# Kernel tuning notes

Measured on AMD Instinct MI355X. Metric: run time of the kernel, lower is better.

Reference implementation:

```python
import jax, jax.numpy as jnp
import numpy as np


def setup_inputs() -> dict:
    key = jax.random.key(0)
    k1, k2, k3, k4 = jax.random.split(key, 4)
    B, L1, L2, H, A = 64, 512, 512, 1024, 1024
    reps_lt = jax.random.normal(k1, (B, L1, H), dtype=jnp.float32)
    reps_rt = jax.random.normal(k2, (B, L2, H), dtype=jnp.float32)
    mask_lt = jnp.ones((B, L1), dtype=jnp.float32)
    mask_rt = jnp.ones((B, L2), dtype=jnp.float32)
    # Keras 'uniform' initializer ~ U(-0.05, 0.05); scale similarly
    attn_w1 = jax.random.uniform(k3, (H, A), dtype=jnp.float32, minval=-0.05, maxval=0.05)
    diagonal_W = jax.random.uniform(k4, (1, 1, A), dtype=jnp.float32, minval=-0.05, maxval=0.05)
    return {
        "reps_lt": reps_lt,
        "reps_rt": reps_rt,
        "mask_lt": mask_lt,
        "mask_rt": mask_rt,
        "attn_w1": attn_w1,
        "diagonal_W": diagonal_W,
    }


def reference(reps_lt, reps_rt, mask_lt, mask_rt, attn_w1, diagonal_W):
    # Projections: the original does expand_dims + broadcast multiply + sum,
    # which is mathematically a matmul over the hidden dim.
    # attn_w2 aliases attn_w1 because hidden dims are equal.
    attn_lt = jnp.tanh(jnp.einsum('blh,ha->bla', reps_lt, attn_w1))  # [B,L1,A]
    attn_rt = jnp.tanh(jnp.einsum('brh,ha->bra', reps_rt, attn_w1))  # [B,L2,A]
    attn_lt = attn_lt * diagonal_W                                   # diagonal bilinear scale
    # batch_dot([B,L1,A], [B,A,L2]) -> [B,L1,L2]
    attn_value = jnp.einsum('bla,bra->blr', attn_lt, attn_rt)
    # mask (multiplicative, as in original) before softmax
    attn_value = attn_value * mask_lt[:, :, None] * mask_rt[:, None, :]
    attn_prob = jax.nn.softmax(attn_value, axis=-1)
    # mask again after softmax
    attn_prob = attn_prob * mask_lt[:, :, None] * mask_rt[:, None, :]
    return attn_prob
```

## Files before the change

kernel.cpp:

```cpp
#include <hip/hip_runtime.h>
#include <hip/hip_bf16.h>

#define B_ 64
#define L_ 512
#define H_ 1024
#define A_ 1024

typedef short bf16x8 __attribute__((ext_vector_type(8)));
typedef float f32x4 __attribute__((ext_vector_type(4)));

__device__ __forceinline__ void gld16(const void* g, void* l) {
  __builtin_amdgcn_global_load_lds((const __attribute__((address_space(1))) void*)g,
                                   (__attribute__((address_space(3))) void*)l, 16, 0, 0);
}

__device__ __forceinline__ unsigned short f2bf(float f) {
  unsigned u = __builtin_bit_cast(unsigned, f);
  u = (u + 0x7fffu + ((u >> 16) & 1u)) >> 16;
  return (unsigned short)u;
}

__device__ __forceinline__ unsigned short cvtbf(float f) {
  __hip_bfloat16 b = __float2bfloat16(f);
  return __builtin_bit_cast(unsigned short, b);
}

__device__ __forceinline__ float fast_tanh(float x) {
  float e = __expf(2.f * x);
  float r = __builtin_amdgcn_rcpf(e + 1.f);
  return __builtin_fmaf(-2.f, r, 1.f);
}

__global__ __launch_bounds__(256) void cvt_kernel(const float* __restrict__ lt,
                                                  const float* __restrict__ rt,
                                                  unsigned short* __restrict__ xb) {
  const size_t NC = (size_t)B_ * L_ * H_ / 8;
  size_t stride = (size_t)gridDim.x * blockDim.x;
  for (size_t c = (size_t)blockIdx.x * blockDim.x + threadIdx.x; c < 2 * NC; c += stride) {
    const float* src = (c < NC) ? (lt + c * 8) : (rt + (c - NC) * 8);
    float4 v0 = ((const float4*)src)[0];
    float4 v1 = ((const float4*)src)[1];
    bf16x8 o;
    o[0] = (short)cvtbf(v0.x); o[1] = (short)cvtbf(v0.y);
    o[2] = (short)cvtbf(v0.z); o[3] = (short)cvtbf(v0.w);
    o[4] = (short)cvtbf(v1.x); o[5] = (short)cvtbf(v1.y);
    o[6] = (short)cvtbf(v1.z); o[7] = (short)cvtbf(v1.w);
    *(bf16x8*)(xb + c * 8) = o;
  }
}

__global__ __launch_bounds__(256) void wtrans_kernel(const float* __restrict__ W,
                                                     unsigned short* __restrict__ Wt) {
  __shared__ float tile[32][33];
  int tx = threadIdx.x & 31, ty = threadIdx.x >> 5;
  int a0 = (blockIdx.x & 31) << 5, h0 = (blockIdx.x >> 5) << 5;
#pragma unroll
  for (int i = 0; i < 4; ++i) {
    int h = ty + i * 8;
    tile[h][tx] = W[(size_t)(h0 + h) * A_ + a0 + tx];
  }
  __syncthreads();
#pragma unroll
  for (int i = 0; i < 4; ++i) {
    int a = ty + i * 8;
    Wt[(size_t)(a0 + a) * H_ + h0 + tx] = f2bf(tile[tx][a]);
  }
}

__global__ __launch_bounds__(512, 2) void proj8_kernel(
    const unsigned short* __restrict__ Xb, const unsigned short* __restrict__ Wt,
    const float* __restrict__ diag, unsigned short* __restrict__ Pb) {
  __shared__ unsigned short As[2][256 * 64];
  __shared__ unsigned short Bs[2][256 * 64];
  int t = threadIdx.x;
  int lane = t & 63, wave = t >> 6;
  int wr = wave >> 2, wc = wave & 3;
  int l15 = lane & 15, l4 = lane >> 4;

  int bid = (int)blockIdx.x;
  int x = bid & 7, k = bid >> 3;
  int mt = x + 8 * (k >> 2);
  int nt = k & 3;
  int mrow0 = mt << 8, ncol0 = nt << 8;
  int isLt = (mt < 128);

  int rs = t >> 3, ss = t & 7;
  const unsigned short* gA = Xb + (size_t)(mrow0 + rs) * H_ + ((ss ^ (rs & 7)) << 3);
  const unsigned short* gB = Wt + (size_t)(ncol0 + rs) * H_ + ((ss ^ (rs & 7)) << 3);
  int lofs = (rs * 8 + ss) * 8;

#define STG_A(buf, h, kt_) {                                              \
    const unsigned short* g_ = gA + (size_t)(h) * 128 * H_ + (kt_) * 64;  \
    gld16(g_, &As[buf][(h) * 8192 + lofs]);                               \
    gld16(g_ + (size_t)64 * H_, &As[buf][(h) * 8192 + 4096 + lofs]); }
#define STG_B(buf, h, kt_) {                                              \
    const unsigned short* g_ = gB + (size_t)(h) * 128 * H_ + (kt_) * 64;  \
    gld16(g_, &Bs[buf][(h) * 8192 + lofs]);                               \
    gld16(g_ + (size_t)64 * H_, &Bs[buf][(h) * 8192 + 4096 + lofs]); }

  int rd0 = (l4 ^ (l15 & 7)) * 8;
  int rd1 = ((4 + l4) ^ (l15 & 7)) * 8;

  f32x4 acc[8][4] = {};
  bf16x8 bq[4][2];

#define LOAD_BQ(buf) { _Pragma("unroll") for (int ni = 0; ni < 4; ++ni) {  \
    int brow = wc * 64 + ni * 16 + l15;                                    \
    bq[ni][0] = *(const bf16x8*)&Bs[buf][brow * 64 + rd0];                 \
    bq[ni][1] = *(const bf16x8*)&Bs[buf][brow * 64 + rd1]; } }

#define PHASE(q, buf, STAGE_OP, CKPT) {                                    \
    bf16x8 aq0, aq1, aq2, aq3;                                             \
    { int ar = wr * 128 + (q) * 32 + l15;                                  \
      aq0 = *(const bf16x8*)&As[buf][ar * 64 + rd0];                       \
      aq1 = *(const bf16x8*)&As[buf][ar * 64 + rd1];                       \
      aq2 = *(const bf16x8*)&As[buf][(ar + 16) * 64 + rd0];                \
      aq3 = *(const bf16x8*)&As[buf][(ar + 16) * 64 + rd1]; }              \
    STAGE_OP;                                                              \
    asm volatile("s_barrier" ::: "memory");                                \
    __builtin_amdgcn_s_setprio(1);                                         \
    _Pragma("unroll") for (int ni = 0; ni < 4; ++ni) {                     \
      acc[(q)*2][ni] = __builtin_amdgcn_mfma_f32_16x16x32_bf16(            \
          aq0, bq[ni][0], acc[(q)*2][ni], 0, 0, 0);                        \
      acc[(q)*2][ni] = __builtin_amdgcn_mfma_f32_16x16x32_bf16(            \
          aq1, bq[ni][1], acc[(q)*2][ni], 0, 0, 0);                        \
      acc[(q)*2+1][ni] = __builtin_amdgcn_mfma_f32_16x16x32_bf16(          \
          aq2, bq[ni][0], acc[(q)*2+1][ni], 0, 0, 0);                      \
      acc[(q)*2+1][ni] = __builtin_amdgcn_mfma_f32_16x16x32_bf16(          \
          aq3, bq[ni][1], acc[(q)*2+1][ni], 0, 0, 0); }                    \
    __builtin_amdgcn_s_setprio(0);                                         \
    if (CKPT) asm volatile("s_waitcnt vmcnt(4)" ::: "memory");             \
    asm volatile("s_barrier" ::: "memory"); }

  STG_B(0, 0, 0); STG_B(0, 1, 0);
  STG_A(0, 0, 0); STG_A(0, 1, 0);
  STG_B(1, 0, 1); STG_B(1, 1, 1);
  asm volatile("s_waitcnt vmcnt(4)" ::: "memory");
  asm volatile("s_barrier" ::: "memory");

  for (int i = 0; i < 8; ++i) {
    int kt1 = 2 * i + 1;
    int kt2 = (2 * i + 2) & 15, kt3 = (2 * i + 3) & 15;
    LOAD_BQ(0);
    PHASE(0, 0, STG_A(1, 0, kt1), 0);
    PHASE(1, 0, STG_A(1, 1, kt1), 0);
    PHASE(2, 0, STG_B(0, 0, kt2), 0);
    PHASE(3, 0, STG_B(0, 1, kt2), 1);
    LOAD_BQ(1);
    PHASE(0, 1, STG_A(0, 0, kt2), 0);
    PHASE(1, 1, STG_A(0, 1, kt2), 0);
    PHASE(2, 1, STG_B(1, 0, kt3), 0);
    PHASE(3, 1, STG_B(1, 1, kt3), 1);
  }
#undef PHASE
#undef LOAD_BQ
#undef STG_A
#undef STG_B

#pragma unroll
  for (int mi = 0; mi < 8; ++mi) {
#pragma unroll
    for (int ni = 0; ni < 4; ++ni) {
      int col = ncol0 + wc * 64 + ni * 16 + l15;
      float d = isLt ? diag[col] : 1.0f;
#pragma unroll
      for (int rr = 0; rr < 4; ++rr) {
        int row = mrow0 + wr * 128 + mi * 16 + l4 * 4 + rr;
        Pb[(size_t)row * A_ + col] = f2bf(fast_tanh(acc[mi][ni][rr]) * d);
      }
    }
  }
}

__global__ __launch_bounds__(256) void score_kernel(
    const unsigned short* __restrict__ Plt, const unsigned short* __restrict__ Prt,
    const float* __restrict__ mask_lt, const float* __restrict__ mask_rt,
    float* __restrict__ out) {
  __shared__ unsigned short As[128 * 64];
  __shared__ unsigned short Bs[128 * 64];
  int t = threadIdx.x;
  int lane = t & 63, wave = t >> 6;
  int wr = wave >> 1, wc = wave & 1;
  int l15 = lane & 15, l4 = lane >> 4;

  int bid = (int)blockIdx.x;
  int x = bid & 7, k = bid >> 3;
  int atile = x + 8 * (k >> 2);
  int b = atile >> 2, tm = atile & 3, tn = k & 3;

  const unsigned short* Abase = Plt + (size_t)b * L_ * A_ + (size_t)(tm * 128) * A_;
  const unsigned short* Bbase = Prt + (size_t)b * L_ * A_ + (size_t)(tn * 128) * A_;

  const unsigned short* asrc[4];
  const unsigned short* bsrc[4];
  int dst[4];
#pragma unroll
  for (int i = 0; i < 4; ++i) {
    int c = i * 256 + t;
    int r = c >> 3, kc = c & 7;
    int sc = (kc ^ (r & 7)) * 8;
    asrc[i] = &Abase[(size_t)r * A_ + sc];
    bsrc[i] = &Bbase[(size_t)r * A_ + sc];
    dst[i] = c * 8;
  }
  int swz0 = ((0 * 4 + l4) ^ (l15 & 7)) * 8;
  int swz1 = ((1 * 4 + l4) ^ (l15 & 7)) * 8;

  f32x4 acc[4][4] = {};
  for (int kt = 0; kt < A_ / 64; ++kt) {
    int k0 = kt * 64;
    __syncthreads();
#pragma unroll
    for (int i = 0; i < 4; ++i) {
      gld16(asrc[i] + k0, &As[dst[i]]);
      gld16(bsrc[i] + k0, &Bs[dst[i]]);
    }
    __syncthreads();
#pragma unroll
    for (int kk = 0; kk < 2; ++kk) {
      int sw = kk ? swz1 : swz0;
      bf16x8 aq[4], bq[4];
#pragma unroll
      for (int mi = 0; mi < 4; ++mi)
        aq[mi] = *(const bf16x8*)&As[(wr * 64 + mi * 16 + l15) * 64 + sw];
#pragma unroll
      for (int ni = 0; ni < 4; ++ni)
        bq[ni] = *(const bf16x8*)&Bs[(wc * 64 + ni * 16 + l15) * 64 + sw];
#pragma unroll
      for (int mi = 0; mi < 4; ++mi)
#pragma unroll
        for (int ni = 0; ni < 4; ++ni)
          acc[mi][ni] = __builtin_amdgcn_mfma_f32_16x16x32_bf16(aq[mi], bq[ni], acc[mi][ni], 0, 0, 0);
    }
  }
  const float* mlp = mask_lt + b * L_;
  const float* mrp = mask_rt + b * L_;
  float* obase = out + (size_t)b * L_ * L_;
#pragma unroll
  for (int mi = 0; mi < 4; ++mi) {
#pragma unroll
    for (int ni = 0; ni < 4; ++ni) {
      int col = tn * 128 + wc * 64 + ni * 16 + l15;
      float mr = mrp[col];
#pragma unroll
      for (int r = 0; r < 4; ++r) {
        int row = tm * 128 + wr * 64 + mi * 16 + l4 * 4 + r;
        obase[(size_t)row * L_ + col] = acc[mi][ni][r] * mlp[row] * mr;
      }
    }
  }
}

__global__ __launch_bounds__(256) void softmax_kernel(float* __restrict__ out,
                                                      const float* __restrict__ mask_lt,
                                                      const float* __restrict__ mask_rt) {
  int lane = threadIdx.x & 63, wave = threadIdx.x >> 6;
  int row = (int)blockIdx.x * 4 + wave;
  int b = row >> 9;
  float* p = out + (size_t)row * L_;
  float4 v0 = *(const float4*)(p + lane * 8);
  float4 v1 = *(const float4*)(p + lane * 8 + 4);
  float m = fmaxf(fmaxf(fmaxf(v0.x, v0.y), fmaxf(v0.z, v0.w)),
                  fmaxf(fmaxf(v1.x, v1.y), fmaxf(v1.z, v1.w)));
#pragma unroll
  for (int off = 32; off; off >>= 1) m = fmaxf(m, __shfl_xor(m, off));
  float e0 = __expf(v0.x - m), e1 = __expf(v0.y - m), e2 = __expf(v0.z - m), e3 = __expf(v0.w - m);
  float e4 = __expf(v1.x - m), e5 = __expf(v1.y - m), e6 = __expf(v1.z - m), e7 = __expf(v1.w - m);
  float s = ((e0 + e1) + (e2 + e3)) + ((e4 + e5) + (e6 + e7));
#pragma unroll
  for (int off = 32; off; off >>= 1) s += __shfl_xor(s, off);
  float sc = (1.0f / s) * mask_lt[row];
  const float* mrp = mask_rt + (b << 9) + lane * 8;
  float4 mr0 = *(const float4*)mrp;
  float4 mr1 = *(const float4*)(mrp + 4);
  float4 o0 = make_float4(e0 * sc * mr0.x, e1 * sc * mr0.y, e2 * sc * mr0.z, e3 * sc * mr0.w);
  float4 o1 = make_float4(e4 * sc * mr1.x, e5 * sc * mr1.y, e6 * sc * mr1.z, e7 * sc * mr1.w);
  *(float4*)(p + lane * 8) = o0;
  *(float4*)(p + lane * 8 + 4) = o1;
}

extern "C" void kernel_launch(void* const* d_in, const int* in_sizes, int n_in,
                              void* d_out, int out_size, void* d_ws, size_t ws_size,
                              hipStream_t stream) {
  const float* reps_lt = (const float*)d_in[0];
  const float* reps_rt = (const float*)d_in[1];
  const float* mask_lt = (const float*)d_in[2];
  const float* mask_rt = (const float*)d_in[3];
  const float* attn_w1 = (const float*)d_in[4];
  const float* diag    = (const float*)d_in[5];
  float* out = (float*)d_out;

  unsigned short* wt  = (unsigned short*)d_ws;
  unsigned short* pb  = wt + (size_t)H_ * A_;
  unsigned short* xb  = pb + (size_t)B_ * L_ * A_ * 2;
  unsigned short* plt = pb;
  unsigned short* prt = pb + (size_t)B_ * L_ * A_;

  hipLaunchKernelGGL(wtrans_kernel, dim3(1024), dim3(256), 0, stream, attn_w1, wt);
  hipLaunchKernelGGL(cvt_kernel, dim3(8192), dim3(256), 0, stream,
                     reps_lt, reps_rt, xb);
  hipLaunchKernelGGL(proj8_kernel, dim3(1024), dim3(512), 0, stream,
                     xb, wt, diag, pb);
  hipLaunchKernelGGL(score_kernel, dim3(1024), dim3(256), 0, stream,
                     plt, prt, mask_lt, mask_rt, out);
  hipLaunchKernelGGL(softmax_kernel, dim3(8192), dim3(256), 0, stream,
                     out, mask_lt, mask_rt);
}
```

Baseline: 315.3 us.

## Reuse pipelined 256x256 MFMA conveyor for the batched score GEMM

The score GEMM moves from a simple 128x128-tile kernel, which syncs twice per k-step, to the 256x256-tile, 512-thread, double-buffered phased pipeline already used by the projection kernel. The pipeline is factored into a shared macro. Larger tiles halve global/LDS traffic per FLOP and overlap loads with MFMA. The cost is only 256 blocks on a GPU with 256 CUs, so each CU gets a single wave of work and occupancy is low.

```diff
diff --git a/kernel.cpp b/kernel.cpp
--- a/kernel.cpp
+++ b/kernel.cpp
@@ -67,55 +67,23 @@
   }
 }
 
-__global__ __launch_bounds__(512, 2) void proj8_kernel(
-    const unsigned short* __restrict__ Xb, const unsigned short* __restrict__ Wt,
-    const float* __restrict__ diag, unsigned short* __restrict__ Pb) {
-  __shared__ unsigned short As[2][256 * 64];
-  __shared__ unsigned short Bs[2][256 * 64];
-  int t = threadIdx.x;
-  int lane = t & 63, wave = t >> 6;
-  int wr = wave >> 2, wc = wave & 3;
-  int l15 = lane & 15, l4 = lane >> 4;
-
-  int bid = (int)blockIdx.x;
-  int x = bid & 7, k = bid >> 3;
-  int mt = x + 8 * (k >> 2);
-  int nt = k & 3;
-  int mrow0 = mt << 8, ncol0 = nt << 8;
-  int isLt = (mt < 128);
-
-  int rs = t >> 3, ss = t & 7;
-  const unsigned short* gA = Xb + (size_t)(mrow0 + rs) * H_ + ((ss ^ (rs & 7)) << 3);
-  const unsigned short* gB = Wt + (size_t)(ncol0 + rs) * H_ + ((ss ^ (rs & 7)) << 3);
-  int lofs = (rs * 8 + ss) * 8;
-
-#define STG_A(buf, h, kt_) {                                              \
-    const unsigned short* g_ = gA + (size_t)(h) * 128 * H_ + (kt_) * 64;  \
-    gld16(g_, &As[buf][(h) * 8192 + lofs]);                               \
-    gld16(g_ + (size_t)64 * H_, &As[buf][(h) * 8192 + 4096 + lofs]); }
-#define STG_B(buf, h, kt_) {                                              \
-    const unsigned short* g_ = gB + (size_t)(h) * 128 * H_ + (kt_) * 64;  \
-    gld16(g_, &Bs[buf][(h) * 8192 + lofs]);                               \
-    gld16(g_ + (size_t)64 * H_, &Bs[buf][(h) * 8192 + 4096 + lofs]); }
-
-  int rd0 = (l4 ^ (l15 & 7)) * 8;
-  int rd1 = ((4 + l4) ^ (l15 & 7)) * 8;
-
-  f32x4 acc[8][4] = {};
-  bf16x8 bq[4][2];
-
-#define LOAD_BQ(buf) { _Pragma("unroll") for (int ni = 0; ni < 4; ++ni) {  \
+#define STG_FROM(gptr, Ls, buf, h, kt_) {                                  \
+    const unsigned short* g_ = (gptr) + (size_t)(h) * 128 * H_ + (kt_) * 64; \
+    gld16(g_, &Ls[buf][(h) * 8192 + lofs]);                                \
+    gld16(g_ + (size_t)64 * H_, &Ls[buf][(h) * 8192 + 4096 + lofs]); }
+
+#define LOAD_BQ(Bsrc, buf) { _Pragma("unroll") for (int ni = 0; ni < 4; ++ni) { \
     int brow = wc * 64 + ni * 16 + l15;                                    \
-    bq[ni][0] = *(const bf16x8*)&Bs[buf][brow * 64 + rd0];                 \
-    bq[ni][1] = *(const bf16x8*)&Bs[buf][brow * 64 + rd1]; } }
-
-#define PHASE(q, buf, STAGE_OP, CKPT) {                                    \
+    bq[ni][0] = *(const bf16x8*)&Bsrc[buf][brow * 64 + rd0];               \
+    bq[ni][1] = *(const bf16x8*)&Bsrc[buf][brow * 64 + rd1]; } }
+
+#define PHASE(Asrc, q, buf, STAGE_OP, CKPT) {                              \
     bf16x8 aq0, aq1, aq2, aq3;                                             \
     { int ar = wr * 128 + (q) * 32 + l15;                                  \
-      aq0 = *(const bf16x8*)&As[buf][ar * 64 + rd0];                       \
-      aq1 = *(const bf16x8*)&As[buf][ar * 64 + rd1];                       \
-      aq2 = *(const bf16x8*)&As[buf][(ar + 16) * 64 + rd0];                \
-      aq3 = *(const bf16x8*)&As[buf][(ar + 16) * 64 + rd1]; }              \
+      aq0 = *(const bf16x8*)&Asrc[buf][ar * 64 + rd0];                     \
+      aq1 = *(const bf16x8*)&Asrc[buf][ar * 64 + rd1];                     \
+      aq2 = *(const bf16x8*)&Asrc[buf][(ar + 16) * 64 + rd0];              \
+      aq3 = *(const bf16x8*)&Asrc[buf][(ar + 16) * 64 + rd1]; }            \
     STAGE_OP;                                                              \
     asm volatile("s_barrier" ::: "memory");                                \
     __builtin_amdgcn_s_setprio(1);                                         \
@@ -132,30 +100,56 @@
     if (CKPT) asm volatile("s_waitcnt vmcnt(4)" ::: "memory");             \
     asm volatile("s_barrier" ::: "memory"); }
 
-  STG_B(0, 0, 0); STG_B(0, 1, 0);
-  STG_A(0, 0, 0); STG_A(0, 1, 0);
-  STG_B(1, 0, 1); STG_B(1, 1, 1);
-  asm volatile("s_waitcnt vmcnt(4)" ::: "memory");
-  asm volatile("s_barrier" ::: "memory");
-
-  for (int i = 0; i < 8; ++i) {
-    int kt1 = 2 * i + 1;
-    int kt2 = (2 * i + 2) & 15, kt3 = (2 * i + 3) & 15;
-    LOAD_BQ(0);
-    PHASE(0, 0, STG_A(1, 0, kt1), 0);
-    PHASE(1, 0, STG_A(1, 1, kt1), 0);
-    PHASE(2, 0, STG_B(0, 0, kt2), 0);
-    PHASE(3, 0, STG_B(0, 1, kt2), 1);
-    LOAD_BQ(1);
-    PHASE(0, 1, STG_A(0, 0, kt2), 0);
-    PHASE(1, 1, STG_A(0, 1, kt2), 0);
-    PHASE(2, 1, STG_B(1, 0, kt3), 0);
-    PHASE(3, 1, STG_B(1, 1, kt3), 1);
-  }
-#undef PHASE
-#undef LOAD_BQ
-#undef STG_A
-#undef STG_B
+#define CONVEYOR(gA_, gB_)                                                 \
+  STG_FROM(gB_, Bs, 0, 0, 0); STG_FROM(gB_, Bs, 0, 1, 0);                  \
+  STG_FROM(gA_, As, 0, 0, 0); STG_FROM(gA_, As, 0, 1, 0);                  \
+  STG_FROM(gB_, Bs, 1, 0, 1); STG_FROM(gB_, Bs, 1, 1, 1);                  \
+  asm volatile("s_waitcnt vmcnt(4)" ::: "memory");                         \
+  asm volatile("s_barrier" ::: "memory");                                  \
+  for (int i = 0; i < 8; ++i) {                                            \
+    int kt1 = 2 * i + 1;                                                   \
+    int kt2 = (2 * i + 2) & 15, kt3 = (2 * i + 3) & 15;                    \
+    LOAD_BQ(Bs, 0);                                                        \
+    PHASE(As, 0, 0, STG_FROM(gA_, As, 1, 0, kt1), 0);                      \
+    PHASE(As, 1, 0, STG_FROM(gA_, As, 1, 1, kt1), 0);                      \
+    PHASE(As, 2, 0, STG_FROM(gB_, Bs, 0, 0, kt2), 0);                      \
+    PHASE(As, 3, 0, STG_FROM(gB_, Bs, 0, 1, kt2), 1);                      \
+    LOAD_BQ(Bs, 1);                                                        \
+    PHASE(As, 0, 1, STG_FROM(gA_, As, 0, 0, kt2), 0);                      \
+    PHASE(As, 1, 1, STG_FROM(gA_, As, 0, 1, kt2), 0);                      \
+    PHASE(As, 2, 1, STG_FROM(gB_, Bs, 1, 0, kt3), 0);                      \
+    PHASE(As, 3, 1, STG_FROM(gB_, Bs, 1, 1, kt3), 1);                      \
+  }
+
+__global__ __launch_bounds__(512, 2) void proj8_kernel(
+    const unsigned short* __restrict__ Xb, const unsigned short* __restrict__ Wt,
+    const float* __restrict__ diag, unsigned short* __restrict__ Pb) {
+  __shared__ unsigned short As[2][256 * 64];
+  __shared__ unsigned short Bs[2][256 * 64];
+  int t = threadIdx.x;
+  int lane = t & 63, wave = t >> 6;
+  int wr = wave >> 2, wc = wave & 3;
+  int l15 = lane & 15, l4 = lane >> 4;
+
+  int bid = (int)blockIdx.x;
+  int x = bid & 7, k = bid >> 3;
+  int mt = x + 8 * (k >> 2);
+  int nt = k & 3;
+  int mrow0 = mt << 8, ncol0 = nt << 8;
+  int isLt = (mt < 128);
+
+  int rs = t >> 3, ss = t & 7;
+  const unsigned short* gA = Xb + (size_t)(mrow0 + rs) * H_ + ((ss ^ (rs & 7)) << 3);
+  const unsigned short* gB = Wt + (size_t)(ncol0 + rs) * H_ + ((ss ^ (rs & 7)) << 3);
+  int lofs = (rs * 8 + ss) * 8;
+
+  int rd0 = (l4 ^ (l15 & 7)) * 8;
+  int rd1 = ((4 + l4) ^ (l15 & 7)) * 8;
+
+  f32x4 acc[8][4] = {};
+  bf16x8 bq[4][2];
+
+  CONVEYOR(gA, gB);
 
 #pragma unroll
   for (int mi = 0; mi < 8; ++mi) {
@@ -172,80 +166,51 @@
   }
 }
 
-__global__ __launch_bounds__(256) void score_kernel(
-    const unsigned short* __restrict__ Plt, const unsigned short* __restrict__ Prt,
+__global__ __launch_bounds__(512, 2) void score8_kernel(
+    const unsigned short* __restrict__ Pb,
     const float* __restrict__ mask_lt, const float* __restrict__ mask_rt,
     float* __restrict__ out) {
-  __shared__ unsigned short As[128 * 64];
-  __shared__ unsigned short Bs[128 * 64];
+  __shared__ unsigned short As[2][256 * 64];
+  __shared__ unsigned short Bs[2][256 * 64];
   int t = threadIdx.x;
   int lane = t & 63, wave = t >> 6;
-  int wr = wave >> 1, wc = wave & 1;
+  int wr = wave >> 2, wc = wave & 3;
   int l15 = lane & 15, l4 = lane >> 4;
 
   int bid = (int)blockIdx.x;
   int x = bid & 7, k = bid >> 3;
-  int atile = x + 8 * (k >> 2);
-  int b = atile >> 2, tm = atile & 3, tn = k & 3;
-
-  const unsigned short* Abase = Plt + (size_t)b * L_ * A_ + (size_t)(tm * 128) * A_;
-  const unsigned short* Bbase = Prt + (size_t)b * L_ * A_ + (size_t)(tn * 128) * A_;
-
-  const unsigned short* asrc[4];
-  const unsigned short* bsrc[4];
-  int dst[4];
-#pragma unroll
-  for (int i = 0; i < 4; ++i) {
-    int c = i * 256 + t;
-    int r = c >> 3, kc = c & 7;
-    int sc = (kc ^ (r & 7)) * 8;
-    asrc[i] = &Abase[(size_t)r * A_ + sc];
-    bsrc[i] = &Bbase[(size_t)r * A_ + sc];
-    dst[i] = c * 8;
-  }
-  int swz0 = ((0 * 4 + l4) ^ (l15 & 7)) * 8;
-  int swz1 = ((1 * 4 + l4) ^ (l15 & 7)) * 8;
-
-  f32x4 acc[4][4] = {};
-  for (int kt = 0; kt < A_ / 64; ++kt) {
-    int k0 = kt * 64;
-    __syncthreads();
-#pragma unroll
-    for (int i = 0; i < 4; ++i) {
-      gld16(asrc[i] + k0, &As[dst[i]]);
-      gld16(bsrc[i] + k0, &Bs[dst[i]]);
-    }
-    __syncthreads();
-#pragma unroll
-    for (int kk = 0; kk < 2; ++kk) {
-      int sw = kk ? swz1 : swz0;
-      bf16x8 aq[4], bq[4];
-#pragma unroll
-      for (int mi = 0; mi < 4; ++mi)
-        aq[mi] = *(const bf16x8*)&As[(wr * 64 + mi * 16 + l15) * 64 + sw];
-#pragma unroll
-      for (int ni = 0; ni < 4; ++ni)
-        bq[ni] = *(const bf16x8*)&Bs[(wc * 64 + ni * 16 + l15) * 64 + sw];
-#pragma unroll
-      for (int mi = 0; mi < 4; ++mi)
-#pragma unroll
-        for (int ni = 0; ni < 4; ++ni)
-          acc[mi][ni] = __builtin_amdgcn_mfma_f32_16x16x32_bf16(aq[mi], bq[ni], acc[mi][ni], 0, 0, 0);
-    }
-  }
+  int pm = x + 8 * (k >> 1);
+  int b = pm >> 1, mt = pm & 1, nt = k & 1;
+
+  int arow0 = b * 512 + mt * 256;
+  int brow0 = 32768 + b * 512 + nt * 256;
+
+  int rs = t >> 3, ss = t & 7;
+  const unsigned short* gA = Pb + (size_t)(arow0 + rs) * H_ + ((ss ^ (rs & 7)) << 3);
+  const unsigned short* gB = Pb + (size_t)(brow0 + rs) * H_ + ((ss ^ (rs & 7)) << 3);
+  int lofs = (rs * 8 + ss) * 8;
+
+  int rd0 = (l4 ^ (l15 & 7)) * 8;
+  int rd1 = ((4 + l4) ^ (l15 & 7)) * 8;
+
+  f32x4 acc[8][4] = {};
+  bf16x8 bq[4][2];
+
+  CONVEYOR(gA, gB);
+
   const float* mlp = mask_lt + b * L_;
   const float* mrp = mask_rt + b * L_;
   float* obase = out + (size_t)b * L_ * L_;
 #pragma unroll
-  for (int mi = 0; mi < 4; ++mi) {
+  for (int mi = 0; mi < 8; ++mi) {
 #pragma unroll
     for (int ni = 0; ni < 4; ++ni) {
-      int col = tn * 128 + wc * 64 + ni * 16 + l15;
+      int col = nt * 256 + wc * 64 + ni * 16 + l15;
       float mr = mrp[col];
 #pragma unroll
-      for (int r = 0; r < 4; ++r) {
-        int row = tm * 128 + wr * 64 + mi * 16 + l4 * 4 + r;
-        obase[(size_t)row * L_ + col] = acc[mi][ni][r] * mlp[row] * mr;
+      for (int rr = 0; rr < 4; ++rr) {
+        int row = mt * 256 + wr * 128 + mi * 16 + l4 * 4 + rr;
+        obase[(size_t)row * L_ + col] = acc[mi][ni][rr] * mlp[row] * mr;
       }
     }
   }
@@ -293,16 +258,14 @@
   unsigned short* wt  = (unsigned short*)d_ws;
   unsigned short* pb  = wt + (size_t)H_ * A_;
   unsigned short* xb  = pb + (size_t)B_ * L_ * A_ * 2;
-  unsigned short* plt = pb;
-  unsigned short* prt = pb + (size_t)B_ * L_ * A_;
 
   hipLaunchKernelGGL(wtrans_kernel, dim3(1024), dim3(256), 0, stream, attn_w1, wt);
   hipLaunchKernelGGL(cvt_kernel, dim3(8192), dim3(256), 0, stream,
                      reps_lt, reps_rt, xb);
   hipLaunchKernelGGL(proj8_kernel, dim3(1024), dim3(512), 0, stream,
                      xb, wt, diag, pb);
-  hipLaunchKernelGGL(score_kernel, dim3(1024), dim3(256), 0, stream,
-                     plt, prt, mask_lt, mask_rt, out);
+  hipLaunchKernelGGL(score8_kernel, dim3(256), dim3(512), 0, stream,
+                     pb, mask_lt, mask_rt, out);
   hipLaunchKernelGGL(softmax_kernel, dim3(8192), dim3(256), 0, stream,
                      out, mask_lt, mask_rt);
 }
```

Measured after the change: 299.3 us. -5.1%, faster.
